# Optimization experiments

Hardware: AMD Instinct MI355X
Metric: run time of the kernel (lower is better)

## Reference

```python
import math
import jax, jax.numpy as jnp
import numpy as np

NUM_BUCKETS = 32
MAX_DISTANCE = 128
HEADS = 16
D_MODEL = 1024
SEQ = 1024
BATCH = 4
SCALE = (D_MODEL // HEADS) ** -0.5  # applied ONLY to the relative-position bias, per the source


def _rel_pos_bucket_causal(seq_len):
    """Causal T5 relative-position bucket: ret[i, j] for query i, key j."""
    pos = jnp.arange(seq_len)
    # rel_pos = k - q ; n = -rel_pos = q - k, clamped at 0 (causal branch)
    n = jnp.maximum(pos[:, None] - pos[None, :], 0)
    max_exact = NUM_BUCKETS // 2  # 16
    # log-spaced buckets for large distances; guard n>=1 to avoid log(0)
    val_large = max_exact + (
        jnp.log(jnp.maximum(n, 1).astype(jnp.float32) / max_exact)
        / math.log(MAX_DISTANCE / max_exact)
        * (NUM_BUCKETS - max_exact)
    ).astype(jnp.int32)
    val_large = jnp.minimum(val_large, NUM_BUCKETS - 1)
    return jnp.where(n < max_exact, n, val_large)  # [i, j] int32


def setup_inputs() -> dict:
    key = jax.random.key(0)
    ks = jax.random.split(key, 6)
    s = 0.02
    return {
        "x": jax.random.normal(ks[0], (BATCH, SEQ, D_MODEL), jnp.float32),
        "Wq": jax.random.normal(ks[1], (D_MODEL, D_MODEL), jnp.float32) * s,
        "bq": jnp.zeros((D_MODEL,), jnp.float32),
        "Wk": jax.random.normal(ks[2], (D_MODEL, D_MODEL), jnp.float32) * s,
        "bk": jnp.zeros((D_MODEL,), jnp.float32),
        "Wv": jax.random.normal(ks[3], (D_MODEL, D_MODEL), jnp.float32) * s,
        "bv": jnp.zeros((D_MODEL,), jnp.float32),
        "Wo": jax.random.normal(ks[4], (D_MODEL, D_MODEL), jnp.float32) * s,
        "bo": jnp.zeros((D_MODEL,), jnp.float32),
        "rel_emb": jax.random.normal(ks[5], (NUM_BUCKETS, HEADS), jnp.float32) * s,
    }


def reference(x, Wq, bq, Wk, bk, Wv, bv, Wo, bo, rel_emb):
    b, n, d = x.shape
    h, hd = HEADS, d // HEADS
    # projections (torch Linear: x @ W^T + b)
    q = (x @ Wq.T + bq).reshape(b, n, h, hd).transpose(0, 2, 1, 3)  # bhnd
    k = (x @ Wk.T + bk).reshape(b, n, h, hd).transpose(0, 2, 1, 3)
    v = (x @ Wv.T + bv).reshape(b, n, h, hd).transpose(0, 2, 1, 3)
    # unscaled dot-product scores (module does not scale q.k)
    sim = jnp.einsum("bhid,bhjd->bhij", q, k)
    # T5 relative-position bias, scaled by head_dim^-0.5
    rp_bucket = _rel_pos_bucket_causal(n)            # [i, j]
    bias = rel_emb[rp_bucket]                        # [i, j, h]
    sim = sim + jnp.transpose(bias, (2, 0, 1)) * SCALE  # broadcast over batch
    # additive causal mask (-inf above diagonal)
    i = jnp.arange(n)
    causal = jnp.where(i[None, :] > i[:, None], -jnp.inf, 0.0).astype(sim.dtype)
    sim = sim + causal
    attn = jax.nn.softmax(sim, axis=-1)
    out = jnp.einsum("bhij,bhjd->bhid", attn, v)
    out = out.transpose(0, 2, 1, 3).reshape(b, n, d)
    return out @ Wo.T + bo
```

## Files before the change

### kernel.cpp

```cpp
#include <hip/hip_runtime.h>
#include <hip/hip_bf16.h>
#include <stdint.h>

#define B_   4
#define SEQ_ 1024
#define DM   1024
#define H_   16
#define HD   64

typedef __bf16 bf16;
typedef __bf16 bf16x8 __attribute__((ext_vector_type(8)));
typedef __bf16 bf16x4v __attribute__((ext_vector_type(4)));
typedef __bf16 bf16x2 __attribute__((ext_vector_type(2)));
typedef float  f32x4 __attribute__((ext_vector_type(4)));

__device__ __forceinline__ void gl_lds16(const void* g, void* s_uniform) {
    __builtin_amdgcn_global_load_lds(
        (const __attribute__((address_space(1))) uint32_t*)g,
        (__attribute__((address_space(3))) uint32_t*)s_uniform,
        16, 0, 0);
}

__global__ __launch_bounds__(256) void prep_kernel(
    const float* __restrict__ x, const float* __restrict__ Wq,
    const float* __restrict__ Wk, const float* __restrict__ Wv,
    const float* __restrict__ Wo, const float* __restrict__ rel,
    bf16* __restrict__ xb, bf16* __restrict__ wqkvb, bf16* __restrict__ wob,
    float* __restrict__ biasT)
{
    int tid = blockIdx.x * 256 + threadIdx.x;
    int stride = gridDim.x * 256;

    for (int i = tid; i < (B_*SEQ_*DM)/4; i += stride) {
        float4 v = ((const float4*)x)[i];
        bf16x4v o; o[0]=(bf16)v.x; o[1]=(bf16)v.y; o[2]=(bf16)v.z; o[3]=(bf16)v.w;
        ((bf16x4v*)xb)[i] = o;
    }
    for (int i = tid; i < (3*DM*DM)/4; i += stride) {
        int n = i >> 8, k4 = i & 255;
        const float* src = (n < 1024) ? Wq : (n < 2048) ? Wk : Wv;
        float4 v = ((const float4*)(src + (size_t)(n & 1023) * DM))[k4];
        bf16x4v o; o[0]=(bf16)v.x; o[1]=(bf16)v.y; o[2]=(bf16)v.z; o[3]=(bf16)v.w;
        ((bf16x4v*)wqkvb)[i] = o;
    }
    for (int i = tid; i < (DM*DM)/4; i += stride) {
        float4 v = ((const float4*)Wo)[i];
        bf16x4v o; o[0]=(bf16)v.x; o[1]=(bf16)v.y; o[2]=(bf16)v.z; o[3]=(bf16)v.w;
        ((bf16x4v*)wob)[i] = o;
    }
    for (int i = tid; i < H_ * SEQ_; i += stride) {
        int h = i >> 10, dist = i & 1023;
        int bkt;
        if (dist < 16) {
            bkt = dist;
        } else {
            float r = logf((float)dist * (1.0f/16.0f)) / logf(8.0f) * 16.0f;
            int vb = 16 + (int)r;
            bkt = vb > 31 ? 31 : vb;
        }
        biasT[i] = rel[bkt * H_ + h] * (0.125f * 1.4426950408889634f);
    }
}

template<int NT>
__global__ __launch_bounds__(256, 3) void gemm_ring(
    const bf16* __restrict__ Ag, const bf16* __restrict__ Bg,
    bf16* __restrict__ qb, bf16* __restrict__ kb, bf16* __restrict__ vtb,
    const float* __restrict__ bq, const float* __restrict__ bk,
    const float* __restrict__ bv)
{
    __shared__ __align__(16) bf16 tile[3][256 * 32];

    const int t = threadIdx.x;
    const int lane = t & 63, w = t >> 6;
    const int wr = w >> 1, wc = w & 1;
    const int row_l = lane & 15;
    const int lg = lane >> 4;

    int xcd = blockIdx.x & 7;
    int idx = blockIdx.x >> 3;
    int ty = (xcd >> 1) * 8 + idx / 12;
    int tx = (xcd & 1) * 12 + idx % 12;
    const int m0 = ty * 128, n0 = tx * 128;

    f32x4 acc[4][4] = {};

    auto STAGE = [&](int buf, int kt) {
        bf16* dst = &tile[buf][0];
        #pragma unroll
        for (int i = 0; i < 4; ++i) {
            int e = i * 2048 + t * 8;
            int r = e >> 5;
            int csw = ((t & 3) ^ (r & 3)) << 3;
            const bf16* src = (r < 128)
                ? (Ag + (long)(m0 + r) * 1024 + kt * 32 + csw)
                : (Bg + (long)(n0 + r - 128) * 1024 + kt * 32 + csw);
            gl_lds16(src, dst + i * 2048 + w * 512);
        }
    };

    auto COMPUTE = [&](int buf) {
        const bf16* bp = &tile[buf][0];
        bf16x8 af[4], bfr[4];
        #pragma unroll
        for (int m = 0; m < 4; ++m) {
            int ra = wr * 64 + m * 16 + row_l;
            af[m] = *(const bf16x8*)&bp[ra * 32 + ((lg ^ (ra & 3)) << 3)];
        }
        #pragma unroll
        for (int n = 0; n < 4; ++n) {
            int rb = 128 + wc * 64 + n * 16 + row_l;
            bfr[n] = *(const bf16x8*)&bp[rb * 32 + ((lg ^ (rb & 3)) << 3)];
        }
        #pragma unroll
        for (int m = 0; m < 4; ++m)
            #pragma unroll
            for (int n = 0; n < 4; ++n)
                acc[m][n] = __builtin_amdgcn_mfma_f32_16x16x32_bf16(
                    af[m], bfr[n], acc[m][n], 0, 0, 0);
    };

    STAGE(0, 0); STAGE(1, 1);
    asm volatile("s_waitcnt vmcnt(4)" ::: "memory");
    __builtin_amdgcn_s_barrier();

    int cb = 0;
    for (int kt = 0; kt < NT; ++kt) {
        int sb = cb - 1; if (sb < 0) sb += 3;
        if (kt + 2 < NT) STAGE(sb, kt + 2);
        COMPUTE(cb);
        if (kt + 2 < NT) { asm volatile("s_waitcnt vmcnt(4)" ::: "memory"); }
        else             { asm volatile("s_waitcnt vmcnt(0)" ::: "memory"); }
        __builtin_amdgcn_s_barrier();
        cb = (cb + 1 == 3) ? 0 : cb + 1;
    }

    const int rbase = (lane >> 4) * 4;

    if (n0 < 2048) {
        #pragma unroll
        for (int m = 0; m < 4; ++m) {
            #pragma unroll
            for (int n = 0; n < 4; ++n) {
                #pragma unroll
                for (int g = 0; g < 4; ++g) {
                    int gm = m0 + wr * 64 + m * 16 + rbase + g;
                    int gn = n0 + wc * 64 + n * 16 + row_l;
                    int which = gn >> 10, nn = gn & 1023;
                    int h = nn >> 6, d = nn & 63;
                    int b = gm >> 10, s = gm & 1023;
                    float v = acc[m][n][g] + ((which == 0) ? bq[nn] : bk[nn]);
                    if (which == 0) v *= 1.4426950408889634f;
                    bf16 bv16 = (bf16)v;
                    if (which == 0)
                        qb[((long)(b*H_ + h)*SEQ_ + s)*HD + d] = bv16;
                    else
                        kb[((long)(b*H_ + h)*SEQ_ + s)*HD + d] = bv16;
                }
            }
        }
    } else {
        bf16* lt = &tile[0][0];
        #pragma unroll
        for (int m = 0; m < 4; ++m) {
            #pragma unroll
            for (int n = 0; n < 4; ++n) {
                int nl = wc * 64 + n * 16 + row_l;
                int mlb = wr * 64 + m * 16 + rbase;
                float bvv = bv[(n0 & 1023) + nl];
                #pragma unroll
                for (int g2 = 0; g2 < 2; ++g2) {
                    bf16x2 pk;
                    pk[0] = (bf16)(acc[m][n][2*g2]     + bvv);
                    pk[1] = (bf16)(acc[m][n][2*g2 + 1] + bvv);
                    int ml = mlb + 2 * g2;
                    int byte = nl * 256 + ((ml * 2) ^ ((nl & 15) << 4));
                    *(bf16x2*)((char*)lt + byte) = pk;
                }
            }
        }
        __syncthreads();
        {
            int nl = t >> 1, sc = t & 1;
            int nn = (n0 & 1023) + nl;
            int h = nn >> 6, d = nn & 63;
            int b = m0 >> 10, s0 = (m0 & 1023) + sc * 64;
            bf16* dst = vtb + ((long)(b*H_ + h)*HD + d)*SEQ_ + s0;
            #pragma unroll
            for (int i = 0; i < 8; ++i) {
                int byte = nl * 256 + ((sc * 128 + i * 16) ^ ((nl & 15) << 4));
                *(float4*)(dst + i * 8) = *(const float4*)((char*)lt + byte);
            }
        }
    }
}

template<int NT>
__global__ __launch_bounds__(256, 2) void gemm_ring_o(
    const bf16* __restrict__ Ag, const bf16* __restrict__ Bg,
    float* __restrict__ outp, const float* __restrict__ bo)
{
    __shared__ __align__(16) bf16 tile[3][192 * 32];

    const int t = threadIdx.x;
    const int lane = t & 63, w = t >> 6;
    const int wr = w >> 1, wc = w & 1;
    const int row_l = lane & 15;
    const int lg = lane >> 4;

    int xcd = blockIdx.x & 7;
    int idx = blockIdx.x >> 3;
    int ty = (xcd >> 1) * 8 + (idx >> 3);
    int tx = (xcd & 1) * 8 + (idx & 7);
    const int m0 = ty * 128, n0 = tx * 64;

    f32x4 acc[4][2] = {};

    auto STAGE = [&](int buf, int kt) {
        bf16* dst = &tile[buf][0];
        #pragma unroll
        for (int i = 0; i < 3; ++i) {
            int e = i * 2048 + t * 8;
            int r = e >> 5;
            int csw = ((t & 3) ^ (r & 3)) << 3;
            const bf16* src = (r < 128)
                ? (Ag + (long)(m0 + r) * 1024 + kt * 32 + csw)
                : (Bg + (long)(n0 + r - 128) * 1024 + kt * 32 + csw);
            gl_lds16(src, dst + i * 2048 + w * 512);
        }
    };

    auto COMPUTE = [&](int buf) {
        const bf16* bp = &tile[buf][0];
        bf16x8 af[4], bfr[2];
        #pragma unroll
        for (int m = 0; m < 4; ++m) {
            int ra = wr * 64 + m * 16 + row_l;
            af[m] = *(const bf16x8*)&bp[ra * 32 + ((lg ^ (ra & 3)) << 3)];
        }
        #pragma unroll
        for (int n = 0; n < 2; ++n) {
            int rb = 128 + wc * 32 + n * 16 + row_l;
            bfr[n] = *(const bf16x8*)&bp[rb * 32 + ((lg ^ (rb & 3)) << 3)];
        }
        #pragma unroll
        for (int m = 0; m < 4; ++m)
            #pragma unroll
            for (int n = 0; n < 2; ++n)
                acc[m][n] = __builtin_amdgcn_mfma_f32_16x16x32_bf16(
                    af[m], bfr[n], acc[m][n], 0, 0, 0);
    };

    STAGE(0, 0); STAGE(1, 1);
    asm volatile("s_waitcnt vmcnt(3)" ::: "memory");
    __builtin_amdgcn_s_barrier();

    int cb = 0;
    for (int kt = 0; kt < NT; ++kt) {
        int sb = cb - 1; if (sb < 0) sb += 3;
        if (kt + 2 < NT) STAGE(sb, kt + 2);
        COMPUTE(cb);
        if (kt + 2 < NT) { asm volatile("s_waitcnt vmcnt(3)" ::: "memory"); }
        else             { asm volatile("s_waitcnt vmcnt(0)" ::: "memory"); }
        __builtin_amdgcn_s_barrier();
        cb = (cb + 1 == 3) ? 0 : cb + 1;
    }

    const int rbase = (lane >> 4) * 4;
    #pragma unroll
    for (int m = 0; m < 4; ++m) {
        #pragma unroll
        for (int n = 0; n < 2; ++n) {
            #pragma unroll
            for (int g = 0; g < 4; ++g) {
                int gm = m0 + wr * 64 + m * 16 + rbase + g;
                int gn = n0 + wc * 32 + n * 16 + row_l;
                outp[(long)gm * DM + gn] = acc[m][n][g] + bo[gn];
            }
        }
    }
}

#define PSTRIDE 72

__global__ __launch_bounds__(512, 4) void attn_kernel(
    const bf16* __restrict__ Qb, const bf16* __restrict__ Kb,
    const bf16* __restrict__ Vtb, const float* __restrict__ biasT,
    bf16* __restrict__ AO)
{
    __shared__ __align__(16) bf16 Ks[2][64 * 64];
    __shared__ __align__(16) bf16 Vs[2][64 * 64];
    __shared__ __align__(16) bf16 Ps[8][16 * PSTRIDE];
    __shared__ float biasS[SEQ_];

    int t = threadIdx.x;
    int lane = t & 63, w = t >> 6;

    int bid = blockIdx.x;
    int xcd = bid & 7;
    int rest = bid >> 3;
    int g = xcd * 8 + (rest & 7);
    int p = rest >> 3;
    int qt_hi = 15 - p;
    int h = g & 15, b = g >> 4;

    int qtw = (w < 4) ? p : qt_hi;
    int row0 = qtw * 64 + (w & 3) * 16;

    int row_l = lane & 15;
    int ksl = (lane >> 4) * 8;
    int rbase = (lane >> 4) * 4;

    const bf16* Kbase = Kb + (long)g * SEQ_ * HD;
    const bf16* Vbase = Vtb + (long)g * HD * SEQ_;

    auto stageKV = [&](int jt) {
        int e = t * 8;
        int r = e >> 6;
        int csw = ((((e >> 3) & 7) ^ (r & 7)) << 3);
        gl_lds16(Kbase + (long)(jt * 64 + r) * HD + csw, &Ks[jt & 1][0] + w * 512);
        gl_lds16(Vbase + (long)r * SEQ_ + jt * 64 + csw, &Vs[jt & 1][0] + w * 512);
    };

    stageKV(0);
    if (t < 256)
        ((float4*)biasS)[t] = ((const float4*)(biasT + (long)h * SEQ_))[t];

    const bf16* Qp = Qb + ((long)g * SEQ_ + row0) * HD;
    bf16x8 qf0 = *(const bf16x8*)&Qp[row_l * HD + ksl];
    bf16x8 qf1 = *(const bf16x8*)&Qp[row_l * HD + 32 + ksl];

    f32x4 oacc[4] = {};
    float lsum[4] = {0.f, 0.f, 0.f, 0.f};
    int ir[4];
    #pragma unroll
    for (int q = 0; q < 4; ++q) ir[q] = row0 + rbase + q;

    for (int jt = 0; jt <= qt_hi; ++jt) {
        asm volatile("s_waitcnt vmcnt(0)" ::: "memory");
        __builtin_amdgcn_s_barrier();
        if (jt < qt_hi) stageKV(jt + 1);

        if (jt <= qtw) {
            const bf16* kb_ = &Ks[jt & 1][0];
            const bf16* vb_ = &Vs[jt & 1][0];

            f32x4 s[4] = {};
            __builtin_amdgcn_s_setprio(1);
            #pragma unroll
            for (int f = 0; f < 4; ++f) {
                int ra = f * 16 + row_l;
                int a0 = (ra * 64 + ksl)      ^ ((ra & 7) << 3);
                int a1 = (ra * 64 + 32 + ksl) ^ ((ra & 7) << 3);
                bf16x8 kf0 = *(const bf16x8*)&kb_[a0];
                bf16x8 kf1 = *(const bf16x8*)&kb_[a1];
                s[f] = __builtin_amdgcn_mfma_f32_16x16x32_bf16(qf0, kf0, s[f], 0,0,0);
                s[f] = __builtin_amdgcn_mfma_f32_16x16x32_bf16(qf1, kf1, s[f], 0,0,0);
            }
            __builtin_amdgcn_s_setprio(0);

            #pragma unroll
            for (int f = 0; f < 4; ++f) {
                int j = jt * 64 + f * 16 + row_l;
                #pragma unroll
                for (int q = 0; q < 4; ++q) {
                    float sv = (j <= ir[q]) ? (s[f][q] + biasS[ir[q] - j]) : -1e30f;
                    float pexp = exp2f(sv);
                    lsum[q] += pexp;
                    Ps[w][(rbase + q) * PSTRIDE + f * 16 + row_l] = (bf16)pexp;
                }
            }
            bf16x8 pf0 = *(const bf16x8*)&Ps[w][row_l * PSTRIDE + ksl];
            bf16x8 pf1 = *(const bf16x8*)&Ps[w][row_l * PSTRIDE + 32 + ksl];

            __builtin_amdgcn_s_setprio(1);
            #pragma unroll
            for (int db = 0; db < 4; ++db) {
                int ra = db * 16 + row_l;
                int a0 = (ra * 64 + ksl)      ^ ((ra & 7) << 3);
                int a1 = (ra * 64 + 32 + ksl) ^ ((ra & 7) << 3);
                bf16x8 vf0 = *(const bf16x8*)&vb_[a0];
                bf16x8 vf1 = *(const bf16x8*)&vb_[a1];
                oacc[db] = __builtin_amdgcn_mfma_f32_16x16x32_bf16(pf0, vf0, oacc[db], 0,0,0);
                oacc[db] = __builtin_amdgcn_mfma_f32_16x16x32_bf16(pf1, vf1, oacc[db], 0,0,0);
            }
            __builtin_amdgcn_s_setprio(0);
        }
    }

    #pragma unroll
    for (int q = 0; q < 4; ++q) {
        float l = lsum[q];
        #pragma unroll
        for (int off = 1; off < 16; off <<= 1) l += __shfl_xor(l, off);
        float inv = 1.0f / l;
        long base = ((long)(b * SEQ_ + ir[q])) * DM + h * HD;
        #pragma unroll
        for (int db = 0; db < 4; ++db)
            AO[base + db * 16 + row_l] = (bf16)(oacc[db][q] * inv);
    }
}

extern "C" void kernel_launch(void* const* d_in, const int* in_sizes, int n_in,
                              void* d_out, int out_size, void* d_ws, size_t ws_size,
                              hipStream_t stream)
{
    const float* x   = (const float*)d_in[0];
    const float* Wq  = (const float*)d_in[1];
    const float* bq  = (const float*)d_in[2];
    const float* Wk  = (const float*)d_in[3];
    const float* bk  = (const float*)d_in[4];
    const float* Wv  = (const float*)d_in[5];
    const float* bv  = (const float*)d_in[6];
    const float* Wo  = (const float*)d_in[7];
    const float* bo  = (const float*)d_in[8];
    const float* rel = (const float*)d_in[9];
    float* out = (float*)d_out;

    char* ws = (char*)d_ws;
    bf16* xb    = (bf16*)ws;  ws += (size_t)B_*SEQ_*DM * 2;
    bf16* wqkvb = (bf16*)ws;  ws += (size_t)3*DM*DM * 2;
    bf16* wob   = (bf16*)ws;  ws += (size_t)DM*DM * 2;
    float* biasT= (float*)ws; ws += (size_t)H_*SEQ_ * 4;
    bf16* Qb    = (bf16*)ws;  ws += (size_t)B_*H_*SEQ_*HD * 2;
    bf16* Kb2   = (bf16*)ws;  ws += (size_t)B_*H_*SEQ_*HD * 2;
    bf16* Vtb   = (bf16*)ws;  ws += (size_t)B_*H_*SEQ_*HD * 2;
    bf16* AO    = (bf16*)ws;  ws += (size_t)B_*SEQ_*DM * 2;

    prep_kernel<<<2048, 256, 0, stream>>>(x, Wq, Wk, Wv, Wo, rel,
                                          xb, wqkvb, wob, biasT);

    gemm_ring<32><<<768, 256, 0, stream>>>(
        xb, wqkvb, Qb, Kb2, Vtb, bq, bk, bv);

    attn_kernel<<<512, 512, 0, stream>>>(Qb, Kb2, Vtb, biasT, AO);

    gemm_ring_o<32><<<512, 256, 0, stream>>>(AO, wob, out, bo);
}
```

Baseline: 98.83 us.

## Enlarge QKV GEMM tiles, triple-buffer attention K/V, swizzle P buffer

The QKV projection GEMM moves to 512-thread blocks with 256x128 tiles, which improves operand reuse per block and halves the grid. The attention kernel goes from double- to triple-buffered K/V staging with a two-tile prefetch distance. It also swaps the padded P scratch for an XOR-swizzled layout, skips the causal mask test on tiles strictly below the diagonal, and rebalances the query-tile-to-block mapping. These changes raise LDS use per block and occupancy pressure, which may lower how many blocks run per CU.

```diff
diff --git a/kernel.cpp b/kernel.cpp
--- a/kernel.cpp
+++ b/kernel.cpp
@@ -63,13 +63,13 @@
 }
 
 template<int NT>
-__global__ __launch_bounds__(256, 3) void gemm_ring(
+__global__ __launch_bounds__(512, 4) void gemm_ring2(
     const bf16* __restrict__ Ag, const bf16* __restrict__ Bg,
     bf16* __restrict__ qb, bf16* __restrict__ kb, bf16* __restrict__ vtb,
     const float* __restrict__ bq, const float* __restrict__ bk,
     const float* __restrict__ bv)
 {
-    __shared__ __align__(16) bf16 tile[3][256 * 32];
+    __shared__ __align__(16) bf16 tile[3][384 * 32];
 
     const int t = threadIdx.x;
     const int lane = t & 63, w = t >> 6;
@@ -79,23 +79,24 @@
 
     int xcd = blockIdx.x & 7;
     int idx = blockIdx.x >> 3;
-    int ty = (xcd >> 1) * 8 + idx / 12;
-    int tx = (xcd & 1) * 12 + idx % 12;
-    const int m0 = ty * 128, n0 = tx * 128;
+    int sub = idx / 24, rem = idx % 24;
+    int ty = (xcd >> 1) * 4 + rem / 6;
+    int tx = (xcd & 1) * 12 + sub * 6 + rem % 6;
+    const int m0 = ty * 256, n0 = tx * 128;
 
     f32x4 acc[4][4] = {};
 
     auto STAGE = [&](int buf, int kt) {
         bf16* dst = &tile[buf][0];
         #pragma unroll
-        for (int i = 0; i < 4; ++i) {
-            int e = i * 2048 + t * 8;
+        for (int i = 0; i < 3; ++i) {
+            int e = i * 4096 + t * 8;
             int r = e >> 5;
             int csw = ((t & 3) ^ (r & 3)) << 3;
-            const bf16* src = (r < 128)
+            const bf16* src = (r < 256)
                 ? (Ag + (long)(m0 + r) * 1024 + kt * 32 + csw)
-                : (Bg + (long)(n0 + r - 128) * 1024 + kt * 32 + csw);
-            gl_lds16(src, dst + i * 2048 + w * 512);
+                : (Bg + (long)(n0 + r - 256) * 1024 + kt * 32 + csw);
+            gl_lds16(src, dst + i * 4096 + w * 512);
         }
     };
 
@@ -109,7 +110,7 @@
         }
         #pragma unroll
         for (int n = 0; n < 4; ++n) {
-            int rb = 128 + wc * 64 + n * 16 + row_l;
+            int rb = 256 + wc * 64 + n * 16 + row_l;
             bfr[n] = *(const bf16x8*)&bp[rb * 32 + ((lg ^ (rb & 3)) << 3)];
         }
         #pragma unroll
@@ -121,7 +122,7 @@
     };
 
     STAGE(0, 0); STAGE(1, 1);
-    asm volatile("s_waitcnt vmcnt(4)" ::: "memory");
+    asm volatile("s_waitcnt vmcnt(3)" ::: "memory");
     __builtin_amdgcn_s_barrier();
 
     int cb = 0;
@@ -129,7 +130,7 @@
         int sb = cb - 1; if (sb < 0) sb += 3;
         if (kt + 2 < NT) STAGE(sb, kt + 2);
         COMPUTE(cb);
-        if (kt + 2 < NT) { asm volatile("s_waitcnt vmcnt(4)" ::: "memory"); }
+        if (kt + 2 < NT) { asm volatile("s_waitcnt vmcnt(3)" ::: "memory"); }
         else             { asm volatile("s_waitcnt vmcnt(0)" ::: "memory"); }
         __builtin_amdgcn_s_barrier();
         cb = (cb + 1 == 3) ? 0 : cb + 1;
@@ -174,21 +175,21 @@
                     pk[0] = (bf16)(acc[m][n][2*g2]     + bvv);
                     pk[1] = (bf16)(acc[m][n][2*g2 + 1] + bvv);
                     int ml = mlb + 2 * g2;
-                    int byte = nl * 256 + ((ml * 2) ^ ((nl & 15) << 4));
+                    int byte = nl * 512 + ((ml * 2) ^ ((nl & 15) << 4));
                     *(bf16x2*)((char*)lt + byte) = pk;
                 }
             }
         }
         __syncthreads();
         {
-            int nl = t >> 1, sc = t & 1;
+            int nl = t >> 2, sc = t & 3;
             int nn = (n0 & 1023) + nl;
             int h = nn >> 6, d = nn & 63;
             int b = m0 >> 10, s0 = (m0 & 1023) + sc * 64;
             bf16* dst = vtb + ((long)(b*H_ + h)*HD + d)*SEQ_ + s0;
             #pragma unroll
             for (int i = 0; i < 8; ++i) {
-                int byte = nl * 256 + ((sc * 128 + i * 16) ^ ((nl & 15) << 4));
+                int byte = nl * 512 + ((sc * 128 + i * 16) ^ ((nl & 15) << 4));
                 *(float4*)(dst + i * 8) = *(const float4*)((char*)lt + byte);
             }
         }
@@ -281,16 +282,14 @@
     }
 }
 
-#define PSTRIDE 72
-
 __global__ __launch_bounds__(512, 4) void attn_kernel(
     const bf16* __restrict__ Qb, const bf16* __restrict__ Kb,
     const bf16* __restrict__ Vtb, const float* __restrict__ biasT,
     bf16* __restrict__ AO)
 {
-    __shared__ __align__(16) bf16 Ks[2][64 * 64];
-    __shared__ __align__(16) bf16 Vs[2][64 * 64];
-    __shared__ __align__(16) bf16 Ps[8][16 * PSTRIDE];
+    __shared__ __align__(16) bf16 Ks[3][64 * 64];
+    __shared__ __align__(16) bf16 Vs[3][64 * 64];
+    __shared__ __align__(16) bf16 Ps[8][16 * 64];
     __shared__ float biasS[SEQ_];
 
     int t = threadIdx.x;
@@ -300,7 +299,8 @@
     int xcd = bid & 7;
     int rest = bid >> 3;
     int g = xcd * 8 + (rest & 7);
-    int p = rest >> 3;
+    int pe = rest >> 3;
+    int p = (pe < 4) ? pe : 11 - pe;
     int qt_hi = 15 - p;
     int h = g & 15, b = g >> 4;
 
@@ -315,14 +315,16 @@
     const bf16* Vbase = Vtb + (long)g * HD * SEQ_;
 
     auto stageKV = [&](int jt) {
+        int sl = jt % 3;
         int e = t * 8;
         int r = e >> 6;
         int csw = ((((e >> 3) & 7) ^ (r & 7)) << 3);
-        gl_lds16(Kbase + (long)(jt * 64 + r) * HD + csw, &Ks[jt & 1][0] + w * 512);
-        gl_lds16(Vbase + (long)r * SEQ_ + jt * 64 + csw, &Vs[jt & 1][0] + w * 512);
+        gl_lds16(Kbase + (long)(jt * 64 + r) * HD + csw, &Ks[sl][0] + w * 512);
+        gl_lds16(Vbase + (long)r * SEQ_ + jt * 64 + csw, &Vs[sl][0] + w * 512);
     };
 
     stageKV(0);
+    stageKV(1);
     if (t < 256)
         ((float4*)biasS)[t] = ((const float4*)(biasT + (long)h * SEQ_))[t];
 
@@ -336,14 +338,21 @@
     #pragma unroll
     for (int q = 0; q < 4; ++q) ir[q] = row0 + rbase + q;
 
+    __syncthreads();
+
+    char* psw = (char*)&Ps[w][0];
+    int prswz = (row_l & 7) << 4;
+
     for (int jt = 0; jt <= qt_hi; ++jt) {
-        asm volatile("s_waitcnt vmcnt(0)" ::: "memory");
+        if (jt < qt_hi) { asm volatile("s_waitcnt vmcnt(2)" ::: "memory"); }
+        else            { asm volatile("s_waitcnt vmcnt(0)" ::: "memory"); }
         __builtin_amdgcn_s_barrier();
-        if (jt < qt_hi) stageKV(jt + 1);
+        if (jt + 2 <= qt_hi) stageKV(jt + 2);
 
         if (jt <= qtw) {
-            const bf16* kb_ = &Ks[jt & 1][0];
-            const bf16* vb_ = &Vs[jt & 1][0];
+            int sl = jt % 3;
+            const bf16* kb_ = &Ks[sl][0];
+            const bf16* vb_ = &Vs[sl][0];
 
             f32x4 s[4] = {};
             __builtin_amdgcn_s_setprio(1);
@@ -359,19 +368,37 @@
             }
             __builtin_amdgcn_s_setprio(0);
 
-            #pragma unroll
-            for (int f = 0; f < 4; ++f) {
-                int j = jt * 64 + f * 16 + row_l;
+            if (jt < qtw) {
                 #pragma unroll
-                for (int q = 0; q < 4; ++q) {
-                    float sv = (j <= ir[q]) ? (s[f][q] + biasS[ir[q] - j]) : -1e30f;
-                    float pexp = exp2f(sv);
-                    lsum[q] += pexp;
-                    Ps[w][(rbase + q) * PSTRIDE + f * 16 + row_l] = (bf16)pexp;
+                for (int f = 0; f < 4; ++f) {
+                    int j = jt * 64 + f * 16 + row_l;
+                    #pragma unroll
+                    for (int q = 0; q < 4; ++q) {
+                        float sv = s[f][q] + biasS[ir[q] - j];
+                        float pexp = exp2f(sv);
+                        lsum[q] += pexp;
+                        int pr = rbase + q;
+                        int byte = pr * 128 + ((((f*16 + row_l) * 2)) ^ ((pr & 7) << 4));
+                        *(bf16*)(psw + byte) = (bf16)pexp;
+                    }
                 }
-            }
-            bf16x8 pf0 = *(const bf16x8*)&Ps[w][row_l * PSTRIDE + ksl];
-            bf16x8 pf1 = *(const bf16x8*)&Ps[w][row_l * PSTRIDE + 32 + ksl];
+            } else {
+                #pragma unroll
+                for (int f = 0; f < 4; ++f) {
+                    int j = jt * 64 + f * 16 + row_l;
+                    #pragma unroll
+                    for (int q = 0; q < 4; ++q) {
+                        float sv = (j <= ir[q]) ? (s[f][q] + biasS[ir[q] - j]) : -1e30f;
+                        float pexp = exp2f(sv);
+                        lsum[q] += pexp;
+                        int pr = rbase + q;
+                        int byte = pr * 128 + ((((f*16 + row_l) * 2)) ^ ((pr & 7) << 4));
+                        *(bf16*)(psw + byte) = (bf16)pexp;
+                    }
+                }
+            }
+            bf16x8 pf0 = *(const bf16x8*)(psw + row_l * 128 + ((ksl * 2) ^ prswz));
+            bf16x8 pf1 = *(const bf16x8*)(psw + row_l * 128 + ((64 + ksl * 2) ^ prswz));
 
             __builtin_amdgcn_s_setprio(1);
             #pragma unroll
@@ -430,7 +457,7 @@
     prep_kernel<<<2048, 256, 0, stream>>>(x, Wq, Wk, Wv, Wo, rel,
                                           xb, wqkvb, wob, biasT);
 
-    gemm_ring<32><<<768, 256, 0, stream>>>(
+    gemm_ring2<32><<<384, 512, 0, stream>>>(
         xb, wqkvb, Qb, Kb2, Vtb, bq, bk, bv);
 
     attn_kernel<<<512, 512, 0, stream>>>(Qb, Kb2, Vtb, biasT, AO);
```

Result: faster. 93.26 us, median of 3 (-5.6%).
